# Optimization experiments

Measured on AMD Instinct MI355X. Metric: run time of the kernel, lower is better.

## Reference

```python
import jax, jax.numpy as jnp
import numpy as np

DIM = 1024
H = 16
HD = DIM // H  # 64
B, N = 2, 2048
EPS = 1e-6


def setup_inputs() -> dict:
    key = jax.random.key(0)
    ks = jax.random.split(key, 12)
    s = 0.02
    return {
        "x": jax.random.normal(ks[0], (B, N, DIM), jnp.float32),
        "rotary_cos": jax.random.uniform(ks[1], (B, N, HD), jnp.float32),
        "rotary_sin": jax.random.uniform(ks[2], (B, N, HD), jnp.float32),
        "Wq": jax.random.normal(ks[3], (DIM, DIM), jnp.float32) * s,
        "bq": jnp.zeros((DIM,), jnp.float32),
        "Wk": jax.random.normal(ks[4], (DIM, DIM), jnp.float32) * s,
        "bk": jnp.zeros((DIM,), jnp.float32),
        "Wv": jax.random.normal(ks[5], (DIM, DIM), jnp.float32) * s,
        "bv": jnp.zeros((DIM,), jnp.float32),
        "q_norm_w": jnp.ones((HD,), jnp.float32),
        "q_norm_b": jnp.zeros((HD,), jnp.float32),
        "k_norm_w": jnp.ones((HD,), jnp.float32),
        "k_norm_b": jnp.zeros((HD,), jnp.float32),
        "Wo": jax.random.normal(ks[6], (DIM, DIM), jnp.float32) * s,
        "bo": jnp.zeros((DIM,), jnp.float32),
    }


def _layernorm(x, w, b):
    mu = jnp.mean(x, axis=-1, keepdims=True)
    var = jnp.mean(jnp.square(x - mu), axis=-1, keepdims=True)
    return (x - mu) * jax.lax.rsqrt(var + EPS) * w + b


def _rotate_half(x):
    x1, x2 = jnp.split(x, 2, axis=-1)
    return jnp.concatenate((-x2, x1), axis=-1)


def _apply_rope(x, cos, sin):
    # x: [B,H,N,D]; cos/sin: [B,N,D] -> [B,1,N,D]
    cos = cos[:, None]
    sin = sin[:, None]
    return x * cos + _rotate_half(x) * sin


def reference(x, rotary_cos, rotary_sin, Wq, bq, Wk, bk, Wv, bv,
              q_norm_w, q_norm_b, k_norm_w, k_norm_b, Wo, bo):
    b, n, c = x.shape
    q = x @ Wq + bq
    k = x @ Wk + bk
    v = x @ Wv + bv
    # Faithful packed-qkv permutation: cat -> view(.., H, 3*hd) -> split(hd)
    qkv = jnp.concatenate((q, k, v), axis=-1).reshape(b, n, H, 3 * HD)
    q, k, v = jnp.split(qkv, 3, axis=-1)  # each [B,N,H,HD]
    q = q.transpose(0, 2, 1, 3)  # [B,H,N,HD]
    k = k.transpose(0, 2, 1, 3)
    v = v.transpose(0, 2, 1, 3)
    q = _layernorm(q, q_norm_w, q_norm_b)
    k = _layernorm(k, k_norm_w, k_norm_b)
    q = _apply_rope(q, rotary_cos, rotary_sin)
    k = _apply_rope(k, rotary_cos, rotary_sin)
    scale = HD ** -0.5
    scores = jnp.einsum("bhqd,bhkd->bhqk", q, k) * scale
    probs = jax.nn.softmax(scores, axis=-1)
    out = jnp.einsum("bhqk,bhkd->bhqd", probs, v)
    out = out.transpose(0, 2, 1, 3).reshape(b, n, c)
    return out @ Wo + bo
```

## Files before the change

### kernel.cpp

```cpp
#include <hip/hip_runtime.h>

typedef __attribute__((ext_vector_type(8))) __bf16 bf16x8;
typedef __attribute__((ext_vector_type(4))) float  f32x4;

#define DEV __device__ __forceinline__

DEV void async_copy16(const void* g, void* l) {
  __builtin_amdgcn_global_load_lds((const __attribute__((address_space(1))) void*)g,
                                   (__attribute__((address_space(3))) void*)l, 16, 0, 0);
}

DEV float ldf(const void* p, size_t i, int isbf) {
  if (isbf) {
    unsigned int w = ((unsigned int)((const unsigned short*)p)[i]) << 16;
    float f; __builtin_memcpy(&f, &w, 4); return f;
  }
  return ((const float*)p)[i];
}

DEV int detect_isbf(const unsigned short* __restrict__ x) {
  int bad = 0;
#pragma unroll
  for (int i = 0; i < 64; i++) {
    int e = (x[i] >> 7) & 0xFF;
    bad |= (e >= 0x90) ? 1 : 0;
  }
  return !bad;
}

__global__ __launch_bounds__(256) void prep(const void* __restrict__ Wq,
                                            const void* __restrict__ Wk,
                                            const void* __restrict__ Wv,
                                            const void* __restrict__ Wo,
                                            const void* __restrict__ x,
                                            const void* __restrict__ bq,
                                            const void* __restrict__ bk,
                                            const void* __restrict__ bv,
                                            const void* __restrict__ bo,
                                            __bf16* __restrict__ Wt,
                                            __bf16* __restrict__ Wot,
                                            __bf16* __restrict__ x_bf,
                                            float* __restrict__ bias) {
  __shared__ float tile[32][33];
  const int isbf = detect_isbf((const unsigned short*)x);
  const int tid = threadIdx.x;
  const int z = blockIdx.z;

  if (z < 4) {
    const void* in = (z == 0) ? Wq : (z == 1) ? Wk : (z == 2) ? Wv : Wo;
    __bf16* out = (z < 3) ? (Wt + (size_t)z * 1024 * 1024) : Wot;
    const int tx = tid & 31, ty = tid >> 5;
    const int r0 = blockIdx.y * 32, c0 = blockIdx.x * 32;
#pragma unroll
    for (int i = 0; i < 4; i++) {
      int r = ty + i * 8;
      tile[r][tx] = ldf(in, (size_t)(r0 + r) * 1024 + c0 + tx, isbf);
    }
    __syncthreads();
#pragma unroll
    for (int i = 0; i < 4; i++) {
      int r = ty + i * 8;
      out[(size_t)(c0 + r) * 1024 + r0 + tx] = (__bf16)tile[tx][r];
    }
  } else {
    const int id = blockIdx.y * 32 + blockIdx.x;
    if (!isbf) {
#pragma unroll
      for (int j = 0; j < 4; j++) {
        int idx = id * 1024 + j * 256 + tid;
        float4 f = ((const float4*)x)[idx];
        union { __bf16 h[4]; uint2 u; } pk;
        pk.h[0] = (__bf16)f.x; pk.h[1] = (__bf16)f.y;
        pk.h[2] = (__bf16)f.z; pk.h[3] = (__bf16)f.w;
        ((uint2*)x_bf)[idx] = pk.u;
      }
    }
    if (id < 16) {
      int i = id * 256 + tid;
      if (i < 1024)      bias[i] = ldf(bq, i, isbf);
      else if (i < 2048) bias[i] = ldf(bk, i - 1024, isbf);
      else if (i < 3072) bias[i] = ldf(bv, i - 2048, isbf);
      else               bias[i] = ldf(bo, i - 3072, isbf);
    }
  }
}

template <int DYN, int NT, int ALT>
__global__ __launch_bounds__(256, 3) void gemm_bt(const __bf16* __restrict__ A,
                                                  const __bf16* __restrict__ Aalt,
                                                  const __bf16* __restrict__ Bt,
                                                  const float* __restrict__ bias,
                                                  void* __restrict__ Cout,
                                                  const unsigned short* __restrict__ xdet,
                                                  int M, int N, int K) {
  constexpr int WN = NT / 2;
  constexpr int JB = WN / 16;
  constexpr int NR = NT / 32;
  __shared__ __align__(16) __bf16 As[128 * 64];
  __shared__ __align__(16) __bf16 Bs[NT * 64];
  const int tid = threadIdx.x;
  const int wid = tid >> 6, lane = tid & 63;
  const int m_blk = blockIdx.x * 128, n_blk = blockIdx.y * NT;
  const int wm = (wid & 1) * 64, wn = (wid >> 1) * WN;
  const int l8 = lane >> 3, l7 = lane & 7;
  const int cc = l7 ^ (l8 & 7);
  const int q4 = lane >> 4, l15 = lane & 15;

  int isbf = 1;
  if (DYN || ALT) isbf = detect_isbf(xdet);
  const __bf16* Ap = (ALT && isbf) ? Aalt : A;

  f32x4 acc[4][JB] = {};

  for (int kb = 0; kb < K; kb += 64) {
    __syncthreads();
#pragma unroll
    for (int i = 0; i < 4; i++) {
      int row = i * 32 + wid * 8 + l8;
      async_copy16(Ap + (size_t)(m_blk + row) * K + kb + cc * 8,
                   As + (i * 32 + wid * 8) * 64);
    }
#pragma unroll
    for (int i = 0; i < NR; i++) {
      int row = i * 32 + wid * 8 + l8;
      async_copy16(Bt + (size_t)(n_blk + row) * K + kb + cc * 8,
                   Bs + (i * 32 + wid * 8) * 64);
    }
    __syncthreads();
#pragma unroll
    for (int k0 = 0; k0 < 64; k0 += 32) {
      bf16x8 a[4], b[JB];
#pragma unroll
      for (int i = 0; i < 4; i++) {
        int ra = wm + i * 16 + l15;
        int ba = ra * 8 + (((k0 >> 3) + q4) ^ (ra & 7));
        a[i] = *(const bf16x8*)&As[ba * 8];
      }
#pragma unroll
      for (int j = 0; j < JB; j++) {
        int rb = wn + j * 16 + l15;
        int bb = rb * 8 + (((k0 >> 3) + q4) ^ (rb & 7));
        b[j] = *(const bf16x8*)&Bs[bb * 8];
      }
#pragma unroll
      for (int i = 0; i < 4; i++)
#pragma unroll
        for (int j = 0; j < JB; j++)
          acc[i][j] = __builtin_amdgcn_mfma_f32_16x16x32_bf16(a[i], b[j], acc[i][j], 0, 0, 0);
    }
  }

  float bcol[JB];
#pragma unroll
  for (int j = 0; j < JB; j++) bcol[j] = bias[n_blk + wn + j * 16 + l15];
#pragma unroll
  for (int i = 0; i < 4; i++)
#pragma unroll
    for (int j = 0; j < JB; j++) {
      int col = n_blk + wn + j * 16 + l15;
#pragma unroll
      for (int r = 0; r < 4; r++) {
        int row = m_blk + wm + i * 16 + q4 * 4 + r;
        float v = acc[i][j][r] + bcol[j];
        size_t idx = (size_t)row * N + col;
        if (DYN && !isbf) ((float*)Cout)[idx] = v;
        else              ((__bf16*)Cout)[idx] = (__bf16)v;
      }
    }
}

__global__ __launch_bounds__(256) void ln_rope_v(const __bf16* __restrict__ qkv,
                                                 const void* __restrict__ rcos,
                                                 const void* __restrict__ rsin,
                                                 const void* __restrict__ qw,
                                                 const void* __restrict__ qb,
                                                 const void* __restrict__ kw,
                                                 const void* __restrict__ kb_,
                                                 const unsigned short* __restrict__ xdet,
                                                 __bf16* __restrict__ Qp,
                                                 __bf16* __restrict__ Kp,
                                                 __bf16* __restrict__ Vt) {
  __shared__ __bf16 vt[64][68];
  const int isbf = detect_isbf(xdet);
  const int tid = threadIdx.x, w = tid >> 6, lane = tid & 63;
  const int bh = blockIdx.y, h = bh & 15, b = bh >> 4;
  const int n0 = blockIdx.x * 64;

  float gq = ldf(qw, lane, isbf), bq_ = ldf(qb, lane, isbf);
  float gk = ldf(kw, lane, isbf), bk_ = ldf(kb_, lane, isbf);

  for (int t = 0; t < 16; t++) {
    const int n = n0 + w * 16 + t;
    const size_t tok = (size_t)b * 2048 + n;
    const __bf16* base = qkv + tok * 3072 + h * 192;
    float qv = (float)base[lane], kv = (float)base[64 + lane], vv = (float)base[128 + lane];

    float sq = qv, sk = kv;
#pragma unroll
    for (int m = 1; m < 64; m <<= 1) { sq += __shfl_xor(sq, m, 64); sk += __shfl_xor(sk, m, 64); }
    float muq = sq * (1.0f / 64.0f), muk = sk * (1.0f / 64.0f);
    float tq = qv - muq, tk = kv - muk;
    float vq = tq * tq, vk = tk * tk;
#pragma unroll
    for (int m = 1; m < 64; m <<= 1) { vq += __shfl_xor(vq, m, 64); vk += __shfl_xor(vk, m, 64); }
    float rsq = rsqrtf(vq * (1.0f / 64.0f) + 1e-6f);
    float rsk = rsqrtf(vk * (1.0f / 64.0f) + 1e-6f);
    float qn = tq * rsq * gq + bq_;
    float kn = tk * rsk * gk + bk_;

    float c = ldf(rcos, tok * 64 + lane, isbf), s = ldf(rsin, tok * 64 + lane, isbf);
    float qpart = __shfl_xor(qn, 32, 64), kpart = __shfl_xor(kn, 32, 64);
    float qrh = (lane < 32) ? -qpart : qpart;
    float krh = (lane < 32) ? -kpart : kpart;

    const size_t oidx = ((size_t)bh * 2048 + n) * 64 + lane;
    Qp[oidx] = (__bf16)((qn * c + qrh * s) * 0.1803368801111204f);
    Kp[oidx] = (__bf16)(kn * c + krh * s);
    vt[lane][w * 16 + t] = (__bf16)vv;
  }
  __syncthreads();
  const int row = tid >> 2, qt = tid & 3;
  size_t gbase = (size_t)bh * 64 * 2048 + (size_t)row * 2048 + n0 + qt * 16;
#pragma unroll
  for (int u = 0; u < 4; u++)
    *(uint2*)&Vt[gbase + u * 4] = *(const uint2*)&vt[row][qt * 16 + u * 4];
}

__global__ __launch_bounds__(256, 4) void attn(const __bf16* __restrict__ Qp,
                                               const __bf16* __restrict__ Kp,
                                               const __bf16* __restrict__ Vt,
                                               float* __restrict__ O0,
                                               float* __restrict__ O1,
                                               float* __restrict__ lpart) {
  __shared__ __align__(16) __bf16 sK[2][2048];
  __shared__ __align__(16) __bf16 sV[2][2048];
  __shared__ __align__(16) __bf16 sP[4][1024];

  const int tid = threadIdx.x, wid = tid >> 6, lane = tid & 63;
  const int q4 = lane >> 4, l15 = lane & 15;
  const int bh = blockIdx.y, split = blockIdx.z;
  const int q0w = blockIdx.x * 128 + wid * 32;
  const int kt0 = split * 1024;
  const __bf16* Qb = Qp + (size_t)bh * 2048 * 64;
  const __bf16* Kb = Kp + (size_t)bh * 2048 * 64;
  const __bf16* Vb = Vt + (size_t)bh * 64 * 2048;
  float* Op = split ? O1 : O0;
  __bf16* sPw = &sP[wid][0];
  const int pbase = (q4 >> 1) * 128 + l15 * 8 + (q4 & 1) * 4;

  bf16x8 qf[2][2];
#pragma unroll
  for (int qs = 0; qs < 2; qs++)
#pragma unroll
    for (int c = 0; c < 2; c++)
      qf[qs][c] = *(const bf16x8*)&Qb[(size_t)(q0w + qs * 16 + l15) * 64 + c * 32 + q4 * 8];

  bf16x8 ones8;
#pragma unroll
  for (int i = 0; i < 8; i++) ones8[i] = (__bf16)1.0f;

  f32x4 o[2][4] = {};
  f32x4 l_acc[2] = {};

#define STAGE(kt, bf)                                                                    \
  do {                                                                                   \
    async_copy16(Kb + (size_t)((kt) + (wid >> 1) * 16 + l15) * 64 + (wid & 1) * 32 + q4 * 8, \
                 &sK[bf][wid * 512]);                                                    \
    async_copy16(Vb + (size_t)(wid * 16 + l15) * 2048 + (kt) + q4 * 8,                   \
                 &sV[bf][wid * 512]);                                                    \
  } while (0)

  STAGE(kt0, 0);

  for (int it = 0; it < 32; ++it) {
    const int buf = it & 1;
    __syncthreads();
    if (it < 31) STAGE(kt0 + (it + 1) * 32, buf ^ 1);

    bf16x8 ak[2][2];
#pragma unroll
    for (int ks = 0; ks < 2; ks++)
#pragma unroll
      for (int c = 0; c < 2; c++)
        ak[ks][c] = *(const bf16x8*)&sK[buf][((ks * 2 + c) * 64 + lane) * 8];
    f32x4 sc[2][2];
#pragma unroll
    for (int qs = 0; qs < 2; qs++)
#pragma unroll
      for (int ks = 0; ks < 2; ks++) {
        f32x4 z = {0.f, 0.f, 0.f, 0.f};
        z = __builtin_amdgcn_mfma_f32_16x16x32_bf16(ak[ks][0], qf[qs][0], z, 0, 0, 0);
        z = __builtin_amdgcn_mfma_f32_16x16x32_bf16(ak[ks][1], qf[qs][1], z, 0, 0, 0);
        sc[qs][ks] = z;
      }

#pragma unroll
    for (int qs = 0; qs < 2; qs++)
#pragma unroll
      for (int ks = 0; ks < 2; ks++) {
        uint2 pk;
        {
          float p0 = __builtin_amdgcn_exp2f(sc[qs][ks][0]);
          float p1 = __builtin_amdgcn_exp2f(sc[qs][ks][1]);
          pk.x = __builtin_amdgcn_perm(__builtin_bit_cast(unsigned int, p1),
                                       __builtin_bit_cast(unsigned int, p0), 0x07060302u);
          float p2 = __builtin_amdgcn_exp2f(sc[qs][ks][2]);
          float p3 = __builtin_amdgcn_exp2f(sc[qs][ks][3]);
          pk.y = __builtin_amdgcn_perm(__builtin_bit_cast(unsigned int, p3),
                                       __builtin_bit_cast(unsigned int, p2), 0x07060302u);
        }
        *(uint2*)&sPw[qs * 512 + ks * 256 + pbase] = pk;
      }
    asm volatile("s_waitcnt lgkmcnt(0)" ::: "memory");

    bf16x8 pb[2];
#pragma unroll
    for (int qs = 0; qs < 2; qs++)
      pb[qs] = *(const bf16x8*)&sPw[(qs * 64 + lane) * 8];
#pragma unroll
    for (int qs = 0; qs < 2; qs++)
      l_acc[qs] = __builtin_amdgcn_mfma_f32_16x16x32_bf16(ones8, pb[qs], l_acc[qs], 0, 0, 0);
#pragma unroll
    for (int ds = 0; ds < 4; ds++) {
      bf16x8 av = *(const bf16x8*)&sV[buf][(ds * 64 + lane) * 8];
#pragma unroll
      for (int qs = 0; qs < 2; qs++)
        o[qs][ds] = __builtin_amdgcn_mfma_f32_16x16x32_bf16(av, pb[qs], o[qs][ds], 0, 0, 0);
    }
  }
#undef STAGE

#pragma unroll
  for (int qs = 0; qs < 2; qs++) {
    const int q = q0w + qs * 16 + l15;
    if (q4 == 0) lpart[(size_t)(split * 32 + bh) * 2048 + q] = l_acc[qs][0];
    size_t base = ((size_t)bh * 2048 + q) * 64;
#pragma unroll
    for (int ds = 0; ds < 4; ds++)
      *(f32x4*)&Op[base + ds * 16 + q4 * 4] = o[qs][ds];
  }
}

__global__ __launch_bounds__(256) void combine(const float* __restrict__ O0,
                                               const float* __restrict__ O1,
                                               const float* __restrict__ lpart,
                                               __bf16* __restrict__ Obuf) {
  const int idx = blockIdx.x * 256 + threadIdx.x;
  const int d4 = idx & 15, q = (idx >> 4) & 2047, bh = idx >> 15;
  const int b = bh >> 4, h = bh & 15;
  const size_t po = ((size_t)bh * 2048 + q) * 64 + d4 * 4;
  f32x4 a = *(const f32x4*)&O0[po];
  f32x4 c = *(const f32x4*)&O1[po];
  float l = lpart[(size_t)bh * 2048 + q] + lpart[(size_t)(32 + bh) * 2048 + q];
  float rl = 1.0f / l;
  union { __bf16 h4[4]; uint2 u; } pk;
#pragma unroll
  for (int r = 0; r < 4; r++) pk.h4[r] = (__bf16)((a[r] + c[r]) * rl);
  *(uint2*)&Obuf[((size_t)(b * 2048 + q)) * 1024 + h * 64 + d4 * 4] = pk.u;
}

extern "C" void kernel_launch(void* const* d_in, const int* in_sizes, int n_in,
                              void* d_out, int out_size, void* d_ws, size_t ws_size,
                              hipStream_t stream) {
  const void* x   = d_in[0];
  const void* rc  = d_in[1];
  const void* rs  = d_in[2];
  const void* Wq  = d_in[3];
  const void* bq  = d_in[4];
  const void* Wk  = d_in[5];
  const void* bk  = d_in[6];
  const void* Wv  = d_in[7];
  const void* bv  = d_in[8];
  const void* qnw = d_in[9];
  const void* qnb = d_in[10];
  const void* knw = d_in[11];
  const void* knb = d_in[12];
  const void* Wo  = d_in[13];
  const void* bo  = d_in[14];
  const unsigned short* xdet = (const unsigned short*)x;

  char* ws = (char*)d_ws;
  __bf16* qkv  = (__bf16*)ws;
  float*  O0   = (float*)ws;
  float*  O1   = (float*)(ws + 16777216);
  __bf16* x_bf = (__bf16*)(ws + 25165824);
  __bf16* Qp   = (__bf16*)(ws + 33554432);
  __bf16* Obuf = (__bf16*)(ws + 33554432);
  __bf16* Kp   = (__bf16*)(ws + 41943040);
  __bf16* Vt   = (__bf16*)(ws + 50331648);
  __bf16* Wt   = (__bf16*)(ws + 58720256);
  __bf16* Wot  = (__bf16*)(ws + 65011712);
  float*  bias = (float*)(ws + 67108864);
  float*  lprt = (float*)(ws + 67125248);

  prep<<<dim3(32, 32, 5), 256, 0, stream>>>(Wq, Wk, Wv, Wo, x, bq, bk, bv, bo,
                                            Wt, Wot, x_bf, bias);
  gemm_bt<0, 128, 1><<<dim3(32, 24), 256, 0, stream>>>(x_bf, (const __bf16*)x, Wt, bias,
                                                       qkv, xdet, 4096, 3072, 1024);
  ln_rope_v<<<dim3(32, 32), 256, 0, stream>>>(qkv, rc, rs, qnw, qnb, knw, knb, xdet,
                                              Qp, Kp, Vt);
  attn<<<dim3(16, 32, 2), 256, 0, stream>>>(Qp, Kp, Vt, O0, O1, lprt);
  combine<<<4096, 256, 0, stream>>>(O0, O1, lprt, Obuf);
  gemm_bt<1, 64, 0><<<dim3(32, 16), 256, 0, stream>>>(Obuf, nullptr, Wot, bias + 3072,
                                                      d_out, xdet, 4096, 1024, 1024);
}
```

Baseline: 242.1 us.

## Fuse split-attention combine into output projection GEMM A-tile load

```diff
diff --git a/kernel.cpp b/kernel.cpp
--- a/kernel.cpp
+++ b/kernel.cpp
@@ -85,13 +85,14 @@
   }
 }
 
-template <int DYN, int NT, int ALT>
-__global__ __launch_bounds__(256, 3) void gemm_bt(const __bf16* __restrict__ A,
-                                                  const __bf16* __restrict__ Aalt,
+template <int DYN, int NT, int MODE>
+__global__ __launch_bounds__(256, 3) void gemm_bt(const void* __restrict__ A,
+                                                  const void* __restrict__ Aalt,
                                                   const __bf16* __restrict__ Bt,
                                                   const float* __restrict__ bias,
                                                   void* __restrict__ Cout,
                                                   const unsigned short* __restrict__ xdet,
+                                                  const float* __restrict__ lp,
                                                   int M, int N, int K) {
   constexpr int WN = NT / 2;
   constexpr int JB = WN / 16;
@@ -107,18 +108,44 @@
   const int q4 = lane >> 4, l15 = lane & 15;
 
   int isbf = 1;
-  if (DYN || ALT) isbf = detect_isbf(xdet);
-  const __bf16* Ap = (ALT && isbf) ? Aalt : A;
+  if (DYN || MODE == 1) isbf = detect_isbf(xdet);
+  const __bf16* Ap = (MODE == 1 && isbf) ? (const __bf16*)Aalt : (const __bf16*)A;
 
   f32x4 acc[4][JB] = {};
 
   for (int kb = 0; kb < K; kb += 64) {
     __syncthreads();
-#pragma unroll
-    for (int i = 0; i < 4; i++) {
-      int row = i * 32 + wid * 8 + l8;
-      async_copy16(Ap + (size_t)(m_blk + row) * K + kb + cc * 8,
-                   As + (i * 32 + wid * 8) * 64);
+    if (MODE == 2) {
+      const float* O0f = (const float*)A;
+      const float* O1f = (const float*)Aalt;
+      const int h = kb >> 6;
+#pragma unroll
+      for (int i = 0; i < 4; i++) {
+        int row = i * 32 + wid * 8 + l8;
+        int m = m_blk + row;
+        int b = m >> 11, qloc = m & 2047;
+        size_t bhq = (size_t)(b * 16 + h) * 2048 + qloc;
+        size_t po = bhq * 64 + cc * 8;
+        f32x4 a0 = *(const f32x4*)&O0f[po];
+        f32x4 a1 = *(const f32x4*)&O0f[po + 4];
+        f32x4 c0 = *(const f32x4*)&O1f[po];
+        f32x4 c1 = *(const f32x4*)&O1f[po + 4];
+        float rl = 1.0f / (lp[bhq] + lp[bhq + 32 * 2048]);
+        union { __bf16 h8[8]; uint4 u; } pk;
+#pragma unroll
+        for (int r = 0; r < 4; r++) {
+          pk.h8[r]     = (__bf16)((a0[r] + c0[r]) * rl);
+          pk.h8[4 + r] = (__bf16)((a1[r] + c1[r]) * rl);
+        }
+        *(uint4*)&As[row * 64 + l7 * 8] = pk.u;
+      }
+    } else {
+#pragma unroll
+      for (int i = 0; i < 4; i++) {
+        int row = i * 32 + wid * 8 + l8;
+        async_copy16(Ap + (size_t)(m_blk + row) * K + kb + cc * 8,
+                     As + (i * 32 + wid * 8) * 64);
+      }
     }
 #pragma unroll
     for (int i = 0; i < NR; i++) {
@@ -189,6 +216,7 @@
   float gq = ldf(qw, lane, isbf), bq_ = ldf(qb, lane, isbf);
   float gk = ldf(kw, lane, isbf), bk_ = ldf(kb_, lane, isbf);
 
+#pragma unroll 2
   for (int t = 0; t < 16; t++) {
     const int n = n0 + w * 16 + t;
     const size_t tok = (size_t)b * 2048 + n;
@@ -339,24 +367,6 @@
     for (int ds = 0; ds < 4; ds++)
       *(f32x4*)&Op[base + ds * 16 + q4 * 4] = o[qs][ds];
   }
-}
-
-__global__ __launch_bounds__(256) void combine(const float* __restrict__ O0,
-                                               const float* __restrict__ O1,
-                                               const float* __restrict__ lpart,
-                                               __bf16* __restrict__ Obuf) {
-  const int idx = blockIdx.x * 256 + threadIdx.x;
-  const int d4 = idx & 15, q = (idx >> 4) & 2047, bh = idx >> 15;
-  const int b = bh >> 4, h = bh & 15;
-  const size_t po = ((size_t)bh * 2048 + q) * 64 + d4 * 4;
-  f32x4 a = *(const f32x4*)&O0[po];
-  f32x4 c = *(const f32x4*)&O1[po];
-  float l = lpart[(size_t)bh * 2048 + q] + lpart[(size_t)(32 + bh) * 2048 + q];
-  float rl = 1.0f / l;
-  union { __bf16 h4[4]; uint2 u; } pk;
-#pragma unroll
-  for (int r = 0; r < 4; r++) pk.h4[r] = (__bf16)((a[r] + c[r]) * rl);
-  *(uint2*)&Obuf[((size_t)(b * 2048 + q)) * 1024 + h * 64 + d4 * 4] = pk.u;
 }
 
 extern "C" void kernel_launch(void* const* d_in, const int* in_sizes, int n_in,
@@ -380,27 +390,25 @@
   const unsigned short* xdet = (const unsigned short*)x;
 
   char* ws = (char*)d_ws;
-  __bf16* qkv  = (__bf16*)ws;
-  float*  O0   = (float*)ws;
-  float*  O1   = (float*)(ws + 16777216);
-  __bf16* x_bf = (__bf16*)(ws + 25165824);
-  __bf16* Qp   = (__bf16*)(ws + 33554432);
-  __bf16* Obuf = (__bf16*)(ws + 33554432);
-  __bf16* Kp   = (__bf16*)(ws + 41943040);
-  __bf16* Vt   = (__bf16*)(ws + 50331648);
-  __bf16* Wt   = (__bf16*)(ws + 58720256);
-  __bf16* Wot  = (__bf16*)(ws + 65011712);
-  float*  bias = (float*)(ws + 67108864);
-  float*  lprt = (float*)(ws + 67125248);
+  __bf16* qkv   = (__bf16*)ws;
+  float*  O0    = (float*)ws;
+  float*  O1    = (float*)(ws + 16777216);
+  __bf16* x_bf  = (__bf16*)(ws + 25165824);
+  __bf16* Qp    = (__bf16*)(ws + 33554432);
+  __bf16* Kp    = (__bf16*)(ws + 41943040);
+  __bf16* Vt    = (__bf16*)(ws + 50331648);
+  __bf16* Wt    = (__bf16*)(ws + 58720256);
+  __bf16* Wot   = (__bf16*)(ws + 65011712);
+  float*  bias  = (float*)(ws + 67108864);
+  float*  lprt  = (float*)(ws + 67125248);
 
   prep<<<dim3(32, 32, 5), 256, 0, stream>>>(Wq, Wk, Wv, Wo, x, bq, bk, bv, bo,
                                             Wt, Wot, x_bf, bias);
-  gemm_bt<0, 128, 1><<<dim3(32, 24), 256, 0, stream>>>(x_bf, (const __bf16*)x, Wt, bias,
-                                                       qkv, xdet, 4096, 3072, 1024);
+  gemm_bt<0, 128, 1><<<dim3(32, 24), 256, 0, stream>>>(x_bf, x, Wt, bias,
+                                                       qkv, xdet, nullptr, 4096, 3072, 1024);
   ln_rope_v<<<dim3(32, 32), 256, 0, stream>>>(qkv, rc, rs, qnw, qnb, knw, knb, xdet,
                                               Qp, Kp, Vt);
   attn<<<dim3(16, 32, 2), 256, 0, stream>>>(Qp, Kp, Vt, O0, O1, lprt);
-  combine<<<4096, 256, 0, stream>>>(O0, O1, lprt, Obuf);
-  gemm_bt<1, 64, 0><<<dim3(32, 16), 256, 0, stream>>>(Obuf, nullptr, Wot, bias + 3072,
-                                                      d_out, xdet, 4096, 1024, 1024);
-}
+  gemm_bt<1, 64, 2><<<dim3(32, 16), 256, 0, stream>>>(O0, O1, Wot, bias + 3072,
+                                                      d_out, xdet, lprt, 4096, 1024, 1024);
+}
```

New measurement: 261.0 us. +7.8%, slower.
